# Optimization experiments

Measured on AMD Instinct MI355X. Metric: run time of the kernel, lower is better.

Reference implementation:

```python
import jax, jax.numpy as jnp
import numpy as np

N_OP, N_TASK, N_TENSOR, N_LINK = 4096, 64, 32768, 1024
N_PLACE = N_OP * N_TASK
NODE_H, EDGE_H = 64, 8
RAW_OP, RAW_TASK, RAW_E = 256, 64, 16
ETYPES = ['link', 'prev', 'succ', 'place', 'serve']
N_LAYERS = 6


def setup_inputs():
    key = jax.random.key(0)
    ks = jax.random.split(key, 20)
    f = jnp.float32
    def w(k, shape, fan_in):
        return jax.random.normal(k, shape, f) / np.sqrt(fan_in)
    return {
        'op_feats': jax.random.normal(ks[0], (N_OP, RAW_OP), f),
        'task_feats': jax.random.normal(ks[1], (N_TASK, RAW_TASK), f),
        'tensor_feats': jax.random.normal(ks[2], (N_TENSOR, RAW_E), f),
        'link_feats': jax.random.normal(ks[3], (N_LINK, RAW_E), f),
        'place_feats': jax.random.normal(ks[4], (N_PLACE, RAW_E), f),
        'prev_src': jax.random.randint(ks[5], (N_TENSOR,), 0, N_OP, jnp.int32),
        'prev_dst': jax.random.randint(ks[6], (N_TENSOR,), 0, N_OP, jnp.int32),
        'link_src': jax.random.randint(ks[7], (N_LINK,), 0, N_TASK, jnp.int32),
        'link_dst': jax.random.randint(ks[8], (N_LINK,), 0, N_TASK, jnp.int32),
        'op_W': w(ks[9], (RAW_OP, NODE_H), RAW_OP),
        'op_b': jnp.zeros((NODE_H,), f),
        'task_W': w(ks[10], (RAW_TASK, NODE_H), RAW_TASK),
        'task_b': jnp.zeros((NODE_H,), f),
        # 5 per-etype edge-trans Dense layers, all raw edge dim = RAW_E
        'eW': w(ks[11], (5, RAW_E, EDGE_H), RAW_E),
        'eb': jnp.zeros((5, EDGE_H), f),
        # GConv Dense per (etype, layer): input = NODE_H + EDGE_H = 72
        'gW': w(ks[12], (5, N_LAYERS, NODE_H + EDGE_H, NODE_H), NODE_H + EDGE_H),
        'gb': jnp.zeros((5, N_LAYERS, NODE_H), f),
        'final_W': w(ks[13], (NODE_H + EDGE_H + NODE_H, 1), NODE_H + EDGE_H + NODE_H),
        'final_b': jnp.zeros((1,), f),
    }


def _mean_agg(msgs, dst, num_segments):
    s = jax.ops.segment_sum(msgs, dst, num_segments=num_segments)
    cnt = jax.ops.segment_sum(jnp.ones((msgs.shape[0], 1), msgs.dtype), dst,
                              num_segments=num_segments)
    return s / jnp.maximum(cnt, 1.0)


def _forward(op_feats, task_feats, tensor_feats, link_feats, place_feats,
             op_W, op_b, task_W, task_b, eW, eb, gW, gb, final_W, final_b,
             prev_src, prev_dst, link_src, link_dst):
    elu = jax.nn.elu
    op = elu(op_feats @ op_W + op_b)      # [N_OP, 64]
    task = elu(task_feats @ task_W + task_b)  # [N_TASK, 64]

    raw_e = {'link': link_feats, 'prev': tensor_feats, 'succ': tensor_feats,
             'place': place_feats, 'serve': place_feats}
    ef = {et: elu(raw_e[et] @ eW[i] + eb[i]) for i, et in enumerate(ETYPES)}

    # place edges: complete bipartite, row-major by op (matches final reshape)
    place_src = jnp.repeat(jnp.arange(N_OP, dtype=jnp.int32), N_TASK)
    place_dst = jnp.tile(jnp.arange(N_TASK, dtype=jnp.int32), N_OP)

    # etype -> (src_idx, dst_idx, src_kind, dst_kind)
    topo = {
        'link':  (link_src, link_dst, 'task', 'task'),
        'prev':  (prev_src, prev_dst, 'op', 'op'),
        'succ':  (prev_dst, prev_src, 'op', 'op'),
        'place': (place_src, place_dst, 'op', 'task'),
        'serve': (place_dst, place_src, 'task', 'op'),
    }
    n_nodes = {'op': N_OP, 'task': N_TASK}

    for l in range(N_LAYERS):
        op_dst, task_dst = [], []
        for i, et in enumerate(ETYPES):
            sidx, didx, skind, dkind = topo[et]
            src = op if skind == 'op' else task
            # gather-concat-Dense per edge: [E, 72] @ [72, 64]
            m = jnp.concatenate([src[sidx], ef[et]], axis=1) @ gW[i, l] + gb[i, l]
            o = _mean_agg(m, didx, n_nodes[dkind])
            (op_dst if dkind == 'op' else task_dst).append(o)
        op = elu(op + sum(op_dst) / len(op_dst))
        task = elu(task + sum(task_dst) / len(task_dst))

    # final per-place-edge score: concat(src op, place edge feat, dst task)
    d = jnp.concatenate([op[place_src], ef['place'], task[place_dst]], axis=1)
    d = d @ final_W + final_b  # [N_PLACE, 1]
    return jnp.reshape(d[:, 0], (N_OP, N_TASK))


def reference(op_feats, task_feats, tensor_feats, link_feats, place_feats,
              prev_src, prev_dst, link_src, link_dst,
              op_W, op_b, task_W, task_b, eW, eb, gW, gb, final_W, final_b):
    return _forward(op_feats, task_feats, tensor_feats, link_feats, place_feats,
                    op_W, op_b, task_W, task_b, eW, eb, gW, gb, final_W, final_b,
                    prev_src, prev_dst, link_src, link_dst)
```

## Files before the change

kernel.cpp:

```cpp
#include <hip/hip_runtime.h>
#include <math.h>

#define NOP 4096
#define NTASK 64
#define NTENSOR 32768
#define NLINK 1024
#define NPLACE (NOP*NTASK)
#define CAP 64
#define NOPB 512

enum : int {
  O_CNT_PREV  = 0,
  O_CNT_SUCC  = O_CNT_PREV + NOP,
  O_CNT_LINK  = O_CNT_SUCC + NOP,
  O_SEF_PREV  = O_CNT_LINK + 64,
  O_SEF_SUCC  = O_SEF_PREV + NOP*8,
  O_SEF_LINK  = O_SEF_SUCC + NOP*8,
  O_SEF_PLACE = O_SEF_LINK + 64*8,
  O_SEF_SERVE = O_SEF_PLACE + 64*8,
  O_OP_A      = O_SEF_SERVE + NOP*8,
  O_OP_B      = O_OP_A + NOP*64,
  O_TASK_A    = O_OP_B + NOP*64,
  O_TASK_B    = O_TASK_A + 64*64,
  O_BPLACE    = O_TASK_B + 64*64,
  O_AOP       = O_BPLACE + NPLACE,
  O_CVEC      = O_AOP + NOP,
  O_MOPP      = O_CVEC + 64,
  O_MTPP      = O_MOPP + 2*512*64,
  O_SPLP      = O_MTPP + 2*4*64,
  O_CSRP_PREV = O_SPLP + 256*512,
  O_CSRP_SUCC = O_CSRP_PREV + NOP*CAP,
  O_CSRP_LINK = O_CSRP_SUCC + NOP*CAP,
  O_EFS_PREV  = O_CSRP_LINK + 64*CAP,
  O_EFS_SUCC  = O_EFS_PREV + NOP*CAP*8,
  O_EFS_LINK  = O_EFS_SUCC + NOP*CAP*8,
  O_TOTAL     = O_EFS_LINK + 64*CAP*8
};

__device__ __forceinline__ float elu1(float x) { return x > 0.f ? x : expm1f(x); }

__device__ __forceinline__ void fma4(float4& a, const float s, const float4 w) {
  a.x = fmaf(s, w.x, a.x);
  a.y = fmaf(s, w.y, a.y);
  a.z = fmaf(s, w.z, a.z);
  a.w = fmaf(s, w.w, a.w);
}

__global__ __launch_bounds__(256) void k_embed(
    const float* __restrict__ opA, const float* __restrict__ opW, const float* __restrict__ opb,
    const float* __restrict__ taskA, const float* __restrict__ taskW, const float* __restrict__ taskb,
    float* __restrict__ ws)
{
  const int tid = threadIdx.x;
  const int bid = blockIdx.x;
  if (bid < 256) {
    __shared__ float sW[8192];
    __shared__ float sA[16*260];
    __shared__ float4 red[256];
    const int obase = bid * 16;
    for (int i = tid; i < 4096; i += 256) {
      const int o = i >> 8, k = i & 255;
      sA[o*260 + k] = opA[(size_t)(obase + o)*256 + k];
    }
    const int o = tid >> 4, hq = tid & 15, h0 = hq*4;
    float4 acc = *(const float4*)&opb[h0];
    for (int half = 0; half < 2; ++half) {
      __syncthreads();
      for (int i = tid*4; i < 8192; i += 1024)
        *(float4*)&sW[i] = *(const float4*)&opW[half*8192 + i];
      __syncthreads();
      const float* a = &sA[o*260 + half*128];
      for (int k = 0; k < 128; ++k)
        fma4(acc, a[k], *(const float4*)&sW[k*64 + h0]);
    }
    acc.x = elu1(acc.x); acc.y = elu1(acc.y); acc.z = elu1(acc.z); acc.w = elu1(acc.w);
    *(float4*)&ws[O_OP_A + (size_t)(obase + o)*64 + h0] = acc;
    red[tid] = acc;
    __syncthreads();
    if (tid < 16) {
      float4 s = make_float4(0.f,0.f,0.f,0.f);
      for (int g = 0; g < 16; ++g) {
        float4 v = red[g*16 + tid];
        s.x += v.x; s.y += v.y; s.z += v.z; s.w += v.w;
      }
      *(float4*)&ws[O_MOPP + bid*64 + tid*4] = s;
    }
  } else {
    __shared__ float sA[64*65];
    __shared__ float sW[64*64];
    __shared__ float4 red[256];
    int* ib = (int*)ws;
    for (int i = tid; i < NOP*2 + 64; i += 256) ib[O_CNT_PREV + i] = 0;
    for (int i = tid; i < 4096; i += 256) {
      const int t = i >> 6, k = i & 63;
      sA[t*65 + k] = taskA[i];
    }
    for (int i = tid*4; i < 4096; i += 1024)
      *(float4*)&sW[i] = *(const float4*)&taskW[i];
    __syncthreads();
    const int og = tid >> 4, hq = tid & 15, h0 = hq*4;
    float4 msum = make_float4(0.f,0.f,0.f,0.f);
    for (int tg = 0; tg < 4; ++tg) {
      const int t = tg*16 + og;
      float4 acc = *(const float4*)&taskb[h0];
      const float* a = &sA[t*65];
      for (int k = 0; k < 64; ++k)
        fma4(acc, a[k], *(const float4*)&sW[k*64 + h0]);
      acc.x = elu1(acc.x); acc.y = elu1(acc.y); acc.z = elu1(acc.z); acc.w = elu1(acc.w);
      *(float4*)&ws[O_TASK_A + t*64 + h0] = acc;
      msum.x += acc.x; msum.y += acc.y; msum.z += acc.z; msum.w += acc.w;
    }
    red[tid] = msum;
    __syncthreads();
    if (tid < 16) {
      float4 s = make_float4(0.f,0.f,0.f,0.f);
      for (int g = 0; g < 16; ++g) {
        float4 v = red[g*16 + tid];
        s.x += v.x; s.y += v.y; s.z += v.z; s.w += v.w;
      }
      *(float4*)&ws[O_MTPP + tid*4] = s;
    }
  }
}

__global__ __launch_bounds__(256) void k_edge_place(
    const float* __restrict__ tensor_feats, const float* __restrict__ link_feats,
    const float* __restrict__ place_feats,
    const int* __restrict__ prev_src, const int* __restrict__ prev_dst,
    const int* __restrict__ link_src, const int* __restrict__ link_dst,
    const float* __restrict__ eW, const float* __restrict__ eb,
    const float* __restrict__ finalW, float* __restrict__ ws)
{
  const int tid = threadIdx.x;
  const int bid = blockIdx.x;
  int* ib = (int*)ws;
  if (bid < 128) {
    __shared__ float sEW[384];
    __shared__ float sEB[24];
    for (int i = tid; i < 384; i += 256) sEW[i] = eW[i];
    if (tid < 24) sEB[tid] = eb[tid];
    __syncthreads();
    const int e = bid*256 + tid;
    float raw[16];
    *(float4*)&raw[0]  = *(const float4*)&tensor_feats[(size_t)e*16 + 0];
    *(float4*)&raw[4]  = *(const float4*)&tensor_feats[(size_t)e*16 + 4];
    *(float4*)&raw[8]  = *(const float4*)&tensor_feats[(size_t)e*16 + 8];
    *(float4*)&raw[12] = *(const float4*)&tensor_feats[(size_t)e*16 + 12];
    float efp[8], efs[8];
#pragma unroll
    for (int c = 0; c < 8; ++c) { efp[c] = sEB[8+c]; efs[c] = sEB[16+c]; }
#pragma unroll
    for (int k = 0; k < 16; ++k) {
      const float a = raw[k];
#pragma unroll
      for (int c = 0; c < 8; ++c) {
        efp[c] = fmaf(a, sEW[128 + k*8 + c], efp[c]);
        efs[c] = fmaf(a, sEW[256 + k*8 + c], efs[c]);
      }
    }
#pragma unroll
    for (int c = 0; c < 8; ++c) { efp[c] = elu1(efp[c]); efs[c] = elu1(efs[c]); }
    const int pd = prev_dst[e], ps = prev_src[e];
    {
      int pos = atomicAdd(&ib[O_CNT_PREV + pd], 1);
      if (pos < CAP) {
        ib[O_CSRP_PREV + pd*CAP + pos] = ps;
        float* dst = ws + O_EFS_PREV + ((size_t)pd*CAP + pos)*8;
        *(float4*)&dst[0] = make_float4(efp[0],efp[1],efp[2],efp[3]);
        *(float4*)&dst[4] = make_float4(efp[4],efp[5],efp[6],efp[7]);
      }
    }
    {
      int pos = atomicAdd(&ib[O_CNT_SUCC + ps], 1);
      if (pos < CAP) {
        ib[O_CSRP_SUCC + ps*CAP + pos] = pd;
        float* dst = ws + O_EFS_SUCC + ((size_t)ps*CAP + pos)*8;
        *(float4*)&dst[0] = make_float4(efs[0],efs[1],efs[2],efs[3]);
        *(float4*)&dst[4] = make_float4(efs[4],efs[5],efs[6],efs[7]);
      }
    }
    if (e < NLINK) {
      float rl[16];
      *(float4*)&rl[0]  = *(const float4*)&link_feats[(size_t)e*16 + 0];
      *(float4*)&rl[4]  = *(const float4*)&link_feats[(size_t)e*16 + 4];
      *(float4*)&rl[8]  = *(const float4*)&link_feats[(size_t)e*16 + 8];
      *(float4*)&rl[12] = *(const float4*)&link_feats[(size_t)e*16 + 12];
      float efl[8];
#pragma unroll
      for (int c = 0; c < 8; ++c) efl[c] = sEB[c];
#pragma unroll
      for (int k = 0; k < 16; ++k) {
        const float a = rl[k];
#pragma unroll
        for (int c = 0; c < 8; ++c) efl[c] = fmaf(a, sEW[k*8 + c], efl[c]);
      }
      const int ld = link_dst[e];
      int pos = atomicAdd(&ib[O_CNT_LINK + ld], 1);
      if (pos < CAP) {
        ib[O_CSRP_LINK + ld*CAP + pos] = link_src[e];
        float* dst = ws + O_EFS_LINK + ((size_t)ld*CAP + pos)*8;
        *(float4*)&dst[0] = make_float4(elu1(efl[0]),elu1(efl[1]),elu1(efl[2]),elu1(efl[3]));
        *(float4*)&dst[4] = make_float4(elu1(efl[4]),elu1(efl[5]),elu1(efl[6]),elu1(efl[7]));
      }
    }
  } else {
    __shared__ float sW3[128], sW4[128], sB3[8], sB4[8], sW1[8];
    __shared__ float pl[512];
    const int pbid = bid - 128;
    if (tid < 128) { sW3[tid] = eW[3*128 + tid]; sW4[tid] = eW[4*128 + tid]; }
    if (tid < 8) { sB3[tid] = eb[24+tid]; sB4[tid] = eb[32+tid]; sW1[tid] = finalW[64+tid]; }
    for (int i = tid; i < 512; i += 256) pl[i] = 0.f;
    __syncthreads();
    const int lane = tid & 63;
    const int wave = (pbid*256 + tid) >> 6;
    float pacc[8];
#pragma unroll
    for (int c = 0; c < 8; ++c) pacc[c] = 0.f;
    float* bplace = ws + O_BPLACE;
    float* sserve = ws + O_SEF_SERVE;
    for (int j = 0; j < 4; ++j) {
      const int i = wave*4 + j;
      const int e = i*64 + lane;
      float raw[16];
      *(float4*)&raw[0]  = *(const float4*)&place_feats[(size_t)e*16 + 0];
      *(float4*)&raw[4]  = *(const float4*)&place_feats[(size_t)e*16 + 4];
      *(float4*)&raw[8]  = *(const float4*)&place_feats[(size_t)e*16 + 8];
      *(float4*)&raw[12] = *(const float4*)&place_feats[(size_t)e*16 + 12];
      float efp[8], efs[8];
#pragma unroll
      for (int c = 0; c < 8; ++c) { efp[c] = sB3[c]; efs[c] = sB4[c]; }
#pragma unroll
      for (int k = 0; k < 16; ++k) {
        const float a = raw[k];
#pragma unroll
        for (int c = 0; c < 8; ++c) {
          efp[c] = fmaf(a, sW3[k*8 + c], efp[c]);
          efs[c] = fmaf(a, sW4[k*8 + c], efs[c]);
        }
      }
      float bp = 0.f;
#pragma unroll
      for (int c = 0; c < 8; ++c) {
        efp[c] = elu1(efp[c]);
        efs[c] = elu1(efs[c]);
        bp = fmaf(efp[c], sW1[c], bp);
        pacc[c] += efp[c];
      }
      bplace[e] = bp;
#pragma unroll
      for (int c = 0; c < 8; ++c) {
        float v = efs[c];
        for (int m = 32; m >= 1; m >>= 1) v += __shfl_xor(v, m, 64);
        if (lane == 0) sserve[i*8 + c] = v;
      }
    }
#pragma unroll
    for (int c = 0; c < 8; ++c) atomicAdd(&pl[lane*8 + c], pacc[c]);
    __syncthreads();
    for (int i = tid; i < 512; i += 256) ws[O_SPLP + pbid*512 + i] = pl[i];
  }
}

__global__ __launch_bounds__(256) void k_layer(
    const int l,
    const float* __restrict__ gW, const float* __restrict__ gb,
    const float* __restrict__ finalW,
    const float* __restrict__ op_in, float* __restrict__ op_out,
    const float* __restrict__ task_in, float* __restrict__ task_out,
    float* __restrict__ ws)
{
  __shared__ float smem[12544];
  const int tid = threadIdx.x;
  const int bid = blockIdx.x;
  const int* ib = (const int*)ws;
  const int rpar = l & 1, wpar = 1 - rpar;

  if (bid < NOPB) {
    float* sWp    = smem;
    float* sWs    = smem + 4608;
    float* sWeS   = smem + 9216;
    float* vp     = smem + 9728;
    float* sums_p = smem + 9984;
    float* sums_s = smem + 10528;
    float* sGB    = smem + 11072;
    float* sef    = smem + 11200;
    float* mop    = smem + 11392;
    int* idxp_s   = (int*)(smem + 11456);
    int* idxs_s   = (int*)(smem + 11968);
    int* cp_s     = (int*)(smem + 12480);
    int* cs_s     = (int*)(smem + 12488);

    const int obase = bid*8;
    const float* gWprev  = gW + (size_t)((6  + l)*72)*64;
    const float* gWsucc  = gW + (size_t)((12 + l)*72)*64;
    const float* gWserve = gW + (size_t)((24 + l)*72)*64;

    for (int i = tid*4; i < 4608; i += 1024) {
      *(float4*)&sWp[i] = *(const float4*)&gWprev[i];
      *(float4*)&sWs[i] = *(const float4*)&gWsucc[i];
    }
    if (tid*4 < 512) *(float4*)&sWeS[tid*4] = *(const float4*)&gWserve[4096 + tid*4];
    if (tid < 8) cp_s[tid] = ib[O_CNT_PREV + obase + tid];
    else if (tid < 16) cs_s[tid-8] = ib[O_CNT_SUCC + obase + (tid-8)];
    for (int i = tid; i < 8*CAP; i += 256) {
      const int o = i >> 6, j = i & 63;
      if (j < ib[O_CNT_PREV + obase + o]) idxp_s[i] = ib[O_CSRP_PREV + (obase+o)*CAP + j];
      if (j < ib[O_CNT_SUCC + obase + o]) idxs_s[i] = ib[O_CSRP_SUCC + (obase+o)*CAP + j];
    }
    if (tid < 128) sGB[tid] = (tid < 64) ? gb[(6+l)*64 + tid] : gb[(12+l)*64 + (tid-64)];
    if (tid < 64) mop[tid] = 0.f;
    if (l == 0) {
      if (tid < 128) {
        const bool isP = (tid < 64);
        const int t2 = tid & 63;
        const int o = t2 >> 3, c = t2 & 7;
        const int cnt = min(ib[(isP ? O_CNT_PREV : O_CNT_SUCC) + obase + o], CAP);
        const float* efs = ws + (isP ? O_EFS_PREV : O_EFS_SUCC) + ((size_t)(obase+o)*CAP)*8;
        float s0 = 0.f, s1 = 0.f;
        int j = 0;
        for (; j+1 < cnt; j += 2) { s0 += efs[j*8+c]; s1 += efs[j*8+8+c]; }
        if (j < cnt) s0 += efs[j*8+c];
        const float s = s0 + s1;
        sef[tid] = s;
        ws[(isP ? O_SEF_PREV : O_SEF_SUCC) + obase*8 + t2] = s;
      } else if (tid < 192) {
        sef[tid] = ws[O_SEF_SERVE + obase*8 + (tid-128)];
      }
    } else {
      if (tid < 64)       sef[tid] = ws[O_SEF_PREV + obase*8 + tid];
      else if (tid < 128) sef[tid] = ws[O_SEF_SUCC + obase*8 + (tid-64)];
      else if (tid < 192) sef[tid] = ws[O_SEF_SERVE + obase*8 + (tid-128)];
    }
    {
      const int col = tid & 63, g = tid >> 6;
      const float* mtpp = ws + O_MTPP + rpar*256;
      const int nst = (l == 0) ? 1 : 4;
      float acc = (g == 0) ? gb[(24+l)*64 + col] : 0.f;
      for (int kk = 0; kk < 16; ++kk) {
        const int k = g*16 + kk;
        float mt = 0.f;
        for (int s = 0; s < nst; ++s) mt += mtpp[s*64 + k];
        acc = fmaf(mt*(1.f/64.f), gWserve[k*64 + col], acc);
      }
      vp[g*64 + col] = acc;
    }
    __syncthreads();

    const int wv = tid >> 6, lane = tid & 63;
#pragma unroll
    for (int oo = 0; oo < 2; ++oo) {
      const int o = 2*wv + oo;
      {
        const int pe = min(cp_s[o], CAP);
        float s0=0.f,s1=0.f,s2=0.f,s3=0.f;
        int p = 0;
        for (; p+3 < pe; p += 4) {
          s0 += op_in[(size_t)idxp_s[o*CAP+p  ]*64 + lane];
          s1 += op_in[(size_t)idxp_s[o*CAP+p+1]*64 + lane];
          s2 += op_in[(size_t)idxp_s[o*CAP+p+2]*64 + lane];
          s3 += op_in[(size_t)idxp_s[o*CAP+p+3]*64 + lane];
        }
        for (; p < pe; ++p) s0 += op_in[(size_t)idxp_s[o*CAP+p]*64 + lane];
        sums_p[o*68 + lane] = (s0+s1)+(s2+s3);
      }
      {
        const int pe = min(cs_s[o], CAP);
        float s0=0.f,s1=0.f,s2=0.f,s3=0.f;
        int p = 0;
        for (; p+3 < pe; p += 4) {
          s0 += op_in[(size_t)idxs_s[o*CAP+p  ]*64 + lane];
          s1 += op_in[(size_t)idxs_s[o*CAP+p+1]*64 + lane];
          s2 += op_in[(size_t)idxs_s[o*CAP+p+2]*64 + lane];
          s3 += op_in[(size_t)idxs_s[o*CAP+p+3]*64 + lane];
        }
        for (; p < pe; ++p) s0 += op_in[(size_t)idxs_s[o*CAP+p]*64 + lane];
        sums_s[o*68 + lane] = (s0+s1)+(s2+s3);
      }
    }

    const int oL = tid >> 5, c = (tid & 31)*2;
    const int d  = obase + oL;
    float up0 = 0.f, up1 = 0.f, us0 = 0.f, us1 = 0.f;
    const int cp = cp_s[oL];
    if (cp > 0) {
      float a0 = 0.f, a1 = 0.f;
      for (int k = 0; k < 64; ++k) {
        const float sk = sums_p[oL*68 + k];
        const float2 wv2 = *(const float2*)&sWp[k*64 + c];
        a0 = fmaf(sk, wv2.x, a0);
        a1 = fmaf(sk, wv2.y, a1);
      }
#pragma unroll
      for (int cc = 0; cc < 8; ++cc) {
        const float ev = sef[oL*8 + cc];
        const float2 wv2 = *(const float2*)&sWp[4096 + cc*64 + c];
        a0 = fmaf(ev, wv2.x, a0);
        a1 = fmaf(ev, wv2.y, a1);
      }
      const float r = 1.f/(float)cp;
      up0 = fmaf(a0, r, sGB[c]);
      up1 = fmaf(a1, r, sGB[c+1]);
    }
    const int cs = cs_s[oL];
    if (cs > 0) {
      float a0 = 0.f, a1 = 0.f;
      for (int k = 0; k < 64; ++k) {
        const float sk = sums_s[oL*68 + k];
        const float2 wv2 = *(const float2*)&sWs[k*64 + c];
        a0 = fmaf(sk, wv2.x, a0);
        a1 = fmaf(sk, wv2.y, a1);
      }
#pragma unroll
      for (int cc = 0; cc < 8; ++cc) {
        const float ev = sef[64 + oL*8 + cc];
        const float2 wv2 = *(const float2*)&sWs[4096 + cc*64 + c];
        a0 = fmaf(ev, wv2.x, a0);
        a1 = fmaf(ev, wv2.y, a1);
      }
      const float r = 1.f/(float)cs;
      us0 = fmaf(a0, r, sGB[64 + c]);
      us1 = fmaf(a1, r, sGB[64 + c + 1]);
    }
    float g0, g1;
    {
      const float2 v0 = *(const float2*)&vp[c];
      const float2 v1 = *(const float2*)&vp[64 + c];
      const float2 v2 = *(const float2*)&vp[128 + c];
      const float2 v3 = *(const float2*)&vp[192 + c];
      g0 = (v0.x + v1.x) + (v2.x + v3.x);
      g1 = (v0.y + v1.y) + (v2.y + v3.y);
#pragma unroll
      for (int cc = 0; cc < 8; ++cc) {
        const float ev = sef[128 + oL*8 + cc] * (1.f/64.f);
        const float2 wv2 = *(const float2*)&sWeS[cc*64 + c];
        g0 = fmaf(ev, wv2.x, g0);
        g1 = fmaf(ev, wv2.y, g1);
      }
    }
    const float2 x = *(const float2*)&op_in[(size_t)d*64 + c];
    const float r0 = elu1(x.x + (up0 + us0 + g0)*(1.f/3.f));
    const float r1 = elu1(x.y + (up1 + us1 + g1)*(1.f/3.f));
    if (l < 5) {
      float2 xo; xo.x = r0; xo.y = r1;
      *(float2*)&op_out[(size_t)d*64 + c] = xo;
      atomicAdd(&mop[c],   r0);
      atomicAdd(&mop[c+1], r1);
      __syncthreads();
      if (tid < 64) ws[O_MOPP + wpar*32768 + bid*64 + tid] = mop[tid];
    } else {
      float av = r0*finalW[c] + r1*finalW[c+1];
      av += __shfl_xor(av, 1, 64);
      av += __shfl_xor(av, 2, 64);
      av += __shfl_xor(av, 4, 64);
      av += __shfl_xor(av, 8, 64);
      av += __shfl_xor(av, 16, 64);
      if ((tid & 31) == 0) ws[O_AOP + d] = av;
    }
  } else {
    const int tbase = (bid - NOPB)*16;
    float* sTask  = smem;
    float* sW0    = smem + 4096;
    float* sWe3   = smem + 8704;
    float* vpl    = smem + 9216;
    float* mo4    = smem + 9472;
    float* sums_l = smem + 9728;
    float* sGB0   = smem + 10816;
    float* sefl   = smem + 10880;
    float* sefpl  = smem + 11008;
    float* mtp    = smem + 11136;
    int* idxl_s   = (int*)(smem + 11200);
    int* cl_s     = (int*)(smem + 12224);

    const float* gWlink  = gW + (size_t)(l*72)*64;
    const float* gWplace = gW + (size_t)((18 + l)*72)*64;

    {
      const int col = tid & 63, g = tid >> 6;
      const float* mopp = ws + O_MOPP + rpar*32768;
      const int nso = (l == 0) ? 256 : 512;
      float a0=0.f,a1=0.f,a2=0.f,a3=0.f,a4=0.f,a5=0.f,a6=0.f,a7=0.f;
      for (int s = g; s < nso; s += 32) {
        a0 += mopp[(s+0 )*64 + col];
        a1 += mopp[(s+4 )*64 + col];
        a2 += mopp[(s+8 )*64 + col];
        a3 += mopp[(s+12)*64 + col];
        a4 += mopp[(s+16)*64 + col];
        a5 += mopp[(s+20)*64 + col];
        a6 += mopp[(s+24)*64 + col];
        a7 += mopp[(s+28)*64 + col];
      }
      mo4[g*64 + col] = ((a0+a1)+(a2+a3)) + ((a4+a5)+(a6+a7));
    }
    for (int i = tid*4; i < 4096; i += 1024)
      *(float4*)&sTask[i] = *(const float4*)&task_in[i];
    for (int i = tid*4; i < 4608; i += 1024)
      *(float4*)&sW0[i] = *(const float4*)&gWlink[i];
    if (tid*4 < 512) *(float4*)&sWe3[tid*4] = *(const float4*)&gWplace[4096 + tid*4];
    if (tid < 16) cl_s[tid] = ib[O_CNT_LINK + tbase + tid];
    for (int i = tid; i < 16*CAP; i += 256) {
      const int t = i >> 6, j = i & 63;
      if (j < ib[O_CNT_LINK + tbase + t]) idxl_s[i] = ib[O_CSRP_LINK + (tbase+t)*CAP + j];
    }
    if (tid < 64) { sGB0[tid] = gb[l*64 + tid]; mtp[tid] = 0.f; }
    if (l == 0) {
      if (tid < 128) {
        const int t = tid >> 3, c = tid & 7;
        const int cnt = min(ib[O_CNT_LINK + tbase + t], CAP);
        const float* efs = ws + O_EFS_LINK + ((size_t)(tbase+t)*CAP)*8;
        float s0 = 0.f, s1 = 0.f;
        int j = 0;
        for (; j+1 < cnt; j += 2) { s0 += efs[j*8+c]; s1 += efs[j*8+8+c]; }
        if (j < cnt) s0 += efs[j*8+c];
        const float s = s0 + s1;
        sefl[tid] = s;
        ws[O_SEF_LINK + tbase*8 + tid] = s;
      } else {
        const int idx = tid - 128;
        float s0=0.f,s1=0.f,s2=0.f,s3=0.f;
        for (int r = 0; r < 256; r += 4) {
          s0 += ws[O_SPLP + (r+0)*512 + tbase*8 + idx];
          s1 += ws[O_SPLP + (r+1)*512 + tbase*8 + idx];
          s2 += ws[O_SPLP + (r+2)*512 + tbase*8 + idx];
          s3 += ws[O_SPLP + (r+3)*512 + tbase*8 + idx];
        }
        const float s = (s0+s1)+(s2+s3);
        sefpl[idx] = s;
        ws[O_SEF_PLACE + tbase*8 + idx] = s;
      }
    } else {
      if (tid < 128) sefl[tid] = ws[O_SEF_LINK + tbase*8 + tid];
      else sefpl[tid - 128] = ws[O_SEF_PLACE + tbase*8 + (tid - 128)];
    }
    __syncthreads();
    {
      const int col = tid & 63, g = tid >> 6;
      float acc = (g == 0) ? gb[(18+l)*64 + col] : 0.f;
      for (int kk = 0; kk < 16; ++kk) {
        const int k = g*16 + kk;
        const float mok = (mo4[k] + mo4[64+k]) + (mo4[128+k] + mo4[192+k]);
        acc = fmaf(mok*(1.f/4096.f), gWplace[k*64 + col], acc);
      }
      vpl[g*64 + col] = acc;
    }
    __syncthreads();

    const int wv = tid >> 6, lane = tid & 63;
#pragma unroll
    for (int tt = 0; tt < 4; ++tt) {
      const int t = 4*wv + tt;
      const int pe = min(cl_s[t], CAP);
      float s0=0.f,s1=0.f,s2=0.f,s3=0.f;
      int p = 0;
      for (; p+3 < pe; p += 4) {
        s0 += sTask[idxl_s[t*CAP+p  ]*64 + lane];
        s1 += sTask[idxl_s[t*CAP+p+1]*64 + lane];
        s2 += sTask[idxl_s[t*CAP+p+2]*64 + lane];
        s3 += sTask[idxl_s[t*CAP+p+3]*64 + lane];
      }
      for (; p < pe; ++p) s0 += sTask[idxl_s[t*CAP+p]*64 + lane];
      sums_l[t*68 + lane] = (s0+s1)+(s2+s3);
    }

    const int tL = tid >> 4, h0 = (tid & 15)*4;
    const int tG = tbase + tL;
    float4 ul = make_float4(0.f,0.f,0.f,0.f);
    const int cl2 = cl_s[tL];
    if (cl2 > 0) {
      float4 a = make_float4(0.f,0.f,0.f,0.f);
      for (int k = 0; k < 64; ++k)
        fma4(a, sums_l[tL*68 + k], *(const float4*)&sW0[k*64 + h0]);
#pragma unroll
      for (int cc = 0; cc < 8; ++cc)
        fma4(a, sefl[tL*8 + cc], *(const float4*)&sW0[4096 + cc*64 + h0]);
      const float r = 1.f/(float)cl2;
      ul.x = fmaf(a.x, r, sGB0[h0+0]);
      ul.y = fmaf(a.y, r, sGB0[h0+1]);
      ul.z = fmaf(a.z, r, sGB0[h0+2]);
      ul.w = fmaf(a.w, r, sGB0[h0+3]);
    }
    float4 uq;
    {
      const float4 v0 = *(const float4*)&vpl[h0];
      const float4 v1 = *(const float4*)&vpl[64 + h0];
      const float4 v2 = *(const float4*)&vpl[128 + h0];
      const float4 v3 = *(const float4*)&vpl[192 + h0];
      uq.x = (v0.x+v1.x)+(v2.x+v3.x);
      uq.y = (v0.y+v1.y)+(v2.y+v3.y);
      uq.z = (v0.z+v1.z)+(v2.z+v3.z);
      uq.w = (v0.w+v1.w)+(v2.w+v3.w);
#pragma unroll
      for (int cc = 0; cc < 8; ++cc)
        fma4(uq, sefpl[tL*8 + cc]*(1.f/4096.f), *(const float4*)&sWe3[cc*64 + h0]);
    }
    float4 x = *(const float4*)&sTask[tG*64 + h0];
    x.x = elu1(x.x + (ul.x + uq.x)*0.5f);
    x.y = elu1(x.y + (ul.y + uq.y)*0.5f);
    x.z = elu1(x.z + (ul.z + uq.z)*0.5f);
    x.w = elu1(x.w + (ul.w + uq.w)*0.5f);
    if (l < 5) {
      *(float4*)&task_out[(size_t)tG*64 + h0] = x;
      atomicAdd(&mtp[h0+0], x.x);
      atomicAdd(&mtp[h0+1], x.y);
      atomicAdd(&mtp[h0+2], x.z);
      atomicAdd(&mtp[h0+3], x.w);
      __syncthreads();
      if (tid < 64) ws[O_MTPP + wpar*256 + (bid - NOPB)*64 + tid] = mtp[tid];
    } else {
      const float4 fw = *(const float4*)&finalW[72 + h0];
      float cv = x.x*fw.x + x.y*fw.y + x.z*fw.z + x.w*fw.w;
      cv += __shfl_xor(cv, 1, 64);
      cv += __shfl_xor(cv, 2, 64);
      cv += __shfl_xor(cv, 4, 64);
      cv += __shfl_xor(cv, 8, 64);
      if ((tid & 15) == 0) ws[O_CVEC + tG] = cv;
    }
  }
}

__global__ __launch_bounds__(256) void k_final(
    const float* __restrict__ ws, const float* __restrict__ finalb,
    float* __restrict__ out)
{
  const int e4 = (blockIdx.x*256 + threadIdx.x)*4;
  const int i = e4 >> 6;
  const int t = e4 & 63;
  const float a = ws[O_AOP + i];
  const float fb = finalb[0];
  const float4 bp = *(const float4*)&ws[O_BPLACE + e4];
  const float4 cv = *(const float4*)&ws[O_CVEC + t];
  float4 o4;
  o4.x = a + bp.x + cv.x + fb;
  o4.y = a + bp.y + cv.y + fb;
  o4.z = a + bp.z + cv.z + fb;
  o4.w = a + bp.w + cv.w + fb;
  *(float4*)&out[e4] = o4;
}

extern "C" void kernel_launch(void* const* d_in, const int* in_sizes, int n_in,
                              void* d_out, int out_size, void* d_ws, size_t ws_size,
                              hipStream_t stream)
{
  (void)in_sizes; (void)n_in; (void)out_size;
  if (ws_size < (size_t)O_TOTAL * sizeof(float)) return;

  const float* op_feats     = (const float*)d_in[0];
  const float* task_feats   = (const float*)d_in[1];
  const float* tensor_feats = (const float*)d_in[2];
  const float* link_feats   = (const float*)d_in[3];
  const float* place_feats  = (const float*)d_in[4];
  const int*   prev_src     = (const int*)d_in[5];
  const int*   prev_dst     = (const int*)d_in[6];
  const int*   link_src     = (const int*)d_in[7];
  const int*   link_dst     = (const int*)d_in[8];
  const float* op_W         = (const float*)d_in[9];
  const float* op_b         = (const float*)d_in[10];
  const float* task_W       = (const float*)d_in[11];
  const float* task_b       = (const float*)d_in[12];
  const float* eW           = (const float*)d_in[13];
  const float* eb           = (const float*)d_in[14];
  const float* gW           = (const float*)d_in[15];
  const float* gb           = (const float*)d_in[16];
  const float* finalW       = (const float*)d_in[17];
  const float* finalb       = (const float*)d_in[18];
  float* w = (float*)d_ws;
  float* out = (float*)d_out;

  k_embed<<<257, 256, 0, stream>>>(op_feats, op_W, op_b, task_feats, task_W, task_b, w);
  k_edge_place<<<384, 256, 0, stream>>>(tensor_feats, link_feats, place_feats,
                                        prev_src, prev_dst, link_src, link_dst,
                                        eW, eb, finalW, w);

  for (int l = 0; l < 6; ++l) {
    const float* oin  = w + ((l & 1) ? O_OP_B : O_OP_A);
    float*       oout = w + ((l & 1) ? O_OP_A : O_OP_B);
    const float* tin  = w + ((l & 1) ? O_TASK_B : O_TASK_A);
    float*       tout = w + ((l & 1) ? O_TASK_A : O_TASK_B);
    k_layer<<<NOPB + 4, 256, 0, stream>>>(l, gW, gb, finalW, oin, oout, tin, tout, w);
  }

  k_final<<<256, 256, 0, stream>>>(w, finalb, out);
}
```

Baseline: 194.9 us.

## Merge op embedding with edge/place prep, overlap weight loads with gathers

Measured after the change: 222.2 us. 1.14x slower.

```diff
diff --git a/kernel.cpp b/kernel.cpp
--- a/kernel.cpp
+++ b/kernel.cpp
@@ -46,17 +46,73 @@
   a.w = fmaf(s, w.w, a.w);
 }
 
-__global__ __launch_bounds__(256) void k_embed(
-    const float* __restrict__ opA, const float* __restrict__ opW, const float* __restrict__ opb,
-    const float* __restrict__ taskA, const float* __restrict__ taskW, const float* __restrict__ taskb,
-    float* __restrict__ ws)
+__global__ __launch_bounds__(256) void k_pre(
+    const float* __restrict__ taskA, const float* __restrict__ taskW,
+    const float* __restrict__ taskb, float* __restrict__ ws)
 {
   const int tid = threadIdx.x;
   const int bid = blockIdx.x;
+  if (bid > 0) {
+    int* ib = (int*)ws;
+    for (int i = (bid - 1)*1024 + tid*4; i < NOP*2 + 64; i += 8192) {
+      ib[O_CNT_PREV + i+0] = 0;
+      ib[O_CNT_PREV + i+1] = 0;
+      ib[O_CNT_PREV + i+2] = 0;
+      ib[O_CNT_PREV + i+3] = 0;
+    }
+    return;
+  }
+  __shared__ float sA[64*65];
+  __shared__ float sW[64*64];
+  __shared__ float4 red[256];
+  for (int i = tid; i < 4096; i += 256) {
+    const int t = i >> 6, k = i & 63;
+    sA[t*65 + k] = taskA[i];
+  }
+  for (int i = tid*4; i < 4096; i += 1024)
+    *(float4*)&sW[i] = *(const float4*)&taskW[i];
+  __syncthreads();
+  const int og = tid >> 4, hq = tid & 15, h0 = hq*4;
+  float4 msum = make_float4(0.f,0.f,0.f,0.f);
+  for (int tg = 0; tg < 4; ++tg) {
+    const int t = tg*16 + og;
+    float4 acc = *(const float4*)&taskb[h0];
+    const float* a = &sA[t*65];
+    for (int k = 0; k < 64; ++k)
+      fma4(acc, a[k], *(const float4*)&sW[k*64 + h0]);
+    acc.x = elu1(acc.x); acc.y = elu1(acc.y); acc.z = elu1(acc.z); acc.w = elu1(acc.w);
+    *(float4*)&ws[O_TASK_A + t*64 + h0] = acc;
+    msum.x += acc.x; msum.y += acc.y; msum.z += acc.z; msum.w += acc.w;
+  }
+  red[tid] = msum;
+  __syncthreads();
+  if (tid < 16) {
+    float4 s = make_float4(0.f,0.f,0.f,0.f);
+    for (int g = 0; g < 16; ++g) {
+      float4 v = red[g*16 + tid];
+      s.x += v.x; s.y += v.y; s.z += v.z; s.w += v.w;
+    }
+    *(float4*)&ws[O_MTPP + tid*4] = s;
+  }
+}
+
+__global__ __launch_bounds__(256) void k_prep(
+    const float* __restrict__ opA, const float* __restrict__ opW, const float* __restrict__ opb,
+    const float* __restrict__ tensor_feats, const float* __restrict__ link_feats,
+    const float* __restrict__ place_feats,
+    const int* __restrict__ prev_src, const int* __restrict__ prev_dst,
+    const int* __restrict__ link_src, const int* __restrict__ link_dst,
+    const float* __restrict__ eW, const float* __restrict__ eb,
+    const float* __restrict__ finalW, float* __restrict__ ws)
+{
+  __shared__ float smem[13376];
+  const int tid = threadIdx.x;
+  const int bid = blockIdx.x;
+  int* ib = (int*)ws;
   if (bid < 256) {
-    __shared__ float sW[8192];
-    __shared__ float sA[16*260];
-    __shared__ float4 red[256];
+    float* sW = smem;
+    float* sA = smem + 8192;
+    float4* red = (float4*)(smem + 12352);
     const int obase = bid * 16;
     for (int i = tid; i < 4096; i += 256) {
       const int o = i >> 8, k = i & 255;
@@ -85,62 +141,13 @@
       }
       *(float4*)&ws[O_MOPP + bid*64 + tid*4] = s;
     }
-  } else {
-    __shared__ float sA[64*65];
-    __shared__ float sW[64*64];
-    __shared__ float4 red[256];
-    int* ib = (int*)ws;
-    for (int i = tid; i < NOP*2 + 64; i += 256) ib[O_CNT_PREV + i] = 0;
-    for (int i = tid; i < 4096; i += 256) {
-      const int t = i >> 6, k = i & 63;
-      sA[t*65 + k] = taskA[i];
-    }
-    for (int i = tid*4; i < 4096; i += 1024)
-      *(float4*)&sW[i] = *(const float4*)&taskW[i];
-    __syncthreads();
-    const int og = tid >> 4, hq = tid & 15, h0 = hq*4;
-    float4 msum = make_float4(0.f,0.f,0.f,0.f);
-    for (int tg = 0; tg < 4; ++tg) {
-      const int t = tg*16 + og;
-      float4 acc = *(const float4*)&taskb[h0];
-      const float* a = &sA[t*65];
-      for (int k = 0; k < 64; ++k)
-        fma4(acc, a[k], *(const float4*)&sW[k*64 + h0]);
-      acc.x = elu1(acc.x); acc.y = elu1(acc.y); acc.z = elu1(acc.z); acc.w = elu1(acc.w);
-      *(float4*)&ws[O_TASK_A + t*64 + h0] = acc;
-      msum.x += acc.x; msum.y += acc.y; msum.z += acc.z; msum.w += acc.w;
-    }
-    red[tid] = msum;
-    __syncthreads();
-    if (tid < 16) {
-      float4 s = make_float4(0.f,0.f,0.f,0.f);
-      for (int g = 0; g < 16; ++g) {
-        float4 v = red[g*16 + tid];
-        s.x += v.x; s.y += v.y; s.z += v.z; s.w += v.w;
-      }
-      *(float4*)&ws[O_MTPP + tid*4] = s;
-    }
-  }
-}
-
-__global__ __launch_bounds__(256) void k_edge_place(
-    const float* __restrict__ tensor_feats, const float* __restrict__ link_feats,
-    const float* __restrict__ place_feats,
-    const int* __restrict__ prev_src, const int* __restrict__ prev_dst,
-    const int* __restrict__ link_src, const int* __restrict__ link_dst,
-    const float* __restrict__ eW, const float* __restrict__ eb,
-    const float* __restrict__ finalW, float* __restrict__ ws)
-{
-  const int tid = threadIdx.x;
-  const int bid = blockIdx.x;
-  int* ib = (int*)ws;
-  if (bid < 128) {
-    __shared__ float sEW[384];
-    __shared__ float sEB[24];
+  } else if (bid < 384) {
+    float* sEW = smem;
+    float* sEB = smem + 384;
     for (int i = tid; i < 384; i += 256) sEW[i] = eW[i];
     if (tid < 24) sEB[tid] = eb[tid];
     __syncthreads();
-    const int e = bid*256 + tid;
+    const int e = (bid - 256)*256 + tid;
     float raw[16];
     *(float4*)&raw[0]  = *(const float4*)&tensor_feats[(size_t)e*16 + 0];
     *(float4*)&raw[4]  = *(const float4*)&tensor_feats[(size_t)e*16 + 4];
@@ -163,7 +170,7 @@
     const int pd = prev_dst[e], ps = prev_src[e];
     {
       int pos = atomicAdd(&ib[O_CNT_PREV + pd], 1);
-      if (pos < CAP) {
+      if (pos >= 0 && pos < CAP) {
         ib[O_CSRP_PREV + pd*CAP + pos] = ps;
         float* dst = ws + O_EFS_PREV + ((size_t)pd*CAP + pos)*8;
         *(float4*)&dst[0] = make_float4(efp[0],efp[1],efp[2],efp[3]);
@@ -172,7 +179,7 @@
     }
     {
       int pos = atomicAdd(&ib[O_CNT_SUCC + ps], 1);
-      if (pos < CAP) {
+      if (pos >= 0 && pos < CAP) {
         ib[O_CSRP_SUCC + ps*CAP + pos] = pd;
         float* dst = ws + O_EFS_SUCC + ((size_t)ps*CAP + pos)*8;
         *(float4*)&dst[0] = make_float4(efs[0],efs[1],efs[2],efs[3]);
@@ -196,7 +203,7 @@
       }
       const int ld = link_dst[e];
       int pos = atomicAdd(&ib[O_CNT_LINK + ld], 1);
-      if (pos < CAP) {
+      if (pos >= 0 && pos < CAP) {
         ib[O_CSRP_LINK + ld*CAP + pos] = link_src[e];
         float* dst = ws + O_EFS_LINK + ((size_t)ld*CAP + pos)*8;
         *(float4*)&dst[0] = make_float4(elu1(efl[0]),elu1(efl[1]),elu1(efl[2]),elu1(efl[3]));
@@ -204,9 +211,13 @@
       }
     }
   } else {
-    __shared__ float sW3[128], sW4[128], sB3[8], sB4[8], sW1[8];
-    __shared__ float pl[512];
-    const int pbid = bid - 128;
+    float* sW3 = smem;
+    float* sW4 = smem + 128;
+    float* sB3 = smem + 256;
+    float* sB4 = smem + 264;
+    float* sW1 = smem + 272;
+    float* pl  = smem + 280;
+    const int pbid = bid - 384;
     if (tid < 128) { sW3[tid] = eW[3*128 + tid]; sW4[tid] = eW[4*128 + tid]; }
     if (tid < 8) { sB3[tid] = eb[24+tid]; sB4[tid] = eb[32+tid]; sW1[tid] = finalW[64+tid]; }
     for (int i = tid; i < 512; i += 256) pl[i] = 0.f;
@@ -295,11 +306,17 @@
     const float* gWsucc  = gW + (size_t)((12 + l)*72)*64;
     const float* gWserve = gW + (size_t)((24 + l)*72)*64;
 
-    for (int i = tid*4; i < 4608; i += 1024) {
-      *(float4*)&sWp[i] = *(const float4*)&gWprev[i];
-      *(float4*)&sWs[i] = *(const float4*)&gWsucc[i];
-    }
-    if (tid*4 < 512) *(float4*)&sWeS[tid*4] = *(const float4*)&gWserve[4096 + tid*4];
+    float4 wreg[10];
+#pragma unroll
+    for (int j = 0; j < 10; ++j) {
+      const int i = tid*4 + j*1024;
+      if (i < 9728) {
+        const float* src = (i < 4608) ? &gWprev[i]
+                         : (i < 9216) ? &gWsucc[i - 4608]
+                                      : &gWserve[4096 + (i - 9216)];
+        wreg[j] = *(const float4*)src;
+      }
+    }
     if (tid < 8) cp_s[tid] = ib[O_CNT_PREV + obase + tid];
     else if (tid < 16) cs_s[tid-8] = ib[O_CNT_SUCC + obase + (tid-8)];
     for (int i = tid; i < 8*CAP; i += 256) {
@@ -310,22 +327,7 @@
     if (tid < 128) sGB[tid] = (tid < 64) ? gb[(6+l)*64 + tid] : gb[(12+l)*64 + (tid-64)];
     if (tid < 64) mop[tid] = 0.f;
     if (l == 0) {
-      if (tid < 128) {
-        const bool isP = (tid < 64);
-        const int t2 = tid & 63;
-        const int o = t2 >> 3, c = t2 & 7;
-        const int cnt = min(ib[(isP ? O_CNT_PREV : O_CNT_SUCC) + obase + o], CAP);
-        const float* efs = ws + (isP ? O_EFS_PREV : O_EFS_SUCC) + ((size_t)(obase+o)*CAP)*8;
-        float s0 = 0.f, s1 = 0.f;
-        int j = 0;
-        for (; j+1 < cnt; j += 2) { s0 += efs[j*8+c]; s1 += efs[j*8+8+c]; }
-        if (j < cnt) s0 += efs[j*8+c];
-        const float s = s0 + s1;
-        sef[tid] = s;
-        ws[(isP ? O_SEF_PREV : O_SEF_SUCC) + obase*8 + t2] = s;
-      } else if (tid < 192) {
-        sef[tid] = ws[O_SEF_SERVE + obase*8 + (tid-128)];
-      }
+      if (tid >= 128 && tid < 192) sef[tid] = ws[O_SEF_SERVE + obase*8 + (tid-128)];
     } else {
       if (tid < 64)       sef[tid] = ws[O_SEF_PREV + obase*8 + tid];
       else if (tid < 128) sef[tid] = ws[O_SEF_SUCC + obase*8 + (tid-64)];
@@ -350,33 +352,69 @@
 #pragma unroll
     for (int oo = 0; oo < 2; ++oo) {
       const int o = 2*wv + oo;
-      {
-        const int pe = min(cp_s[o], CAP);
+      const int pep = min(cp_s[o], CAP);
+      const int pes = min(cs_s[o], CAP);
+      const int* ip = &idxp_s[o*CAP];
+      const int* iq = &idxs_s[o*CAP];
+      float p0=0.f,p1=0.f,p2=0.f,p3=0.f,q0=0.f,q1=0.f,q2=0.f,q3=0.f;
+      int p = 0, q = 0;
+      while (p+3 < pep && q+3 < pes) {
+        const int a0=ip[p],a1=ip[p+1],a2=ip[p+2],a3=ip[p+3];
+        const int b0=iq[q],b1=iq[q+1],b2=iq[q+2],b3=iq[q+3];
+        p0 += op_in[(size_t)a0*64 + lane];
+        p1 += op_in[(size_t)a1*64 + lane];
+        p2 += op_in[(size_t)a2*64 + lane];
+        p3 += op_in[(size_t)a3*64 + lane];
+        q0 += op_in[(size_t)b0*64 + lane];
+        q1 += op_in[(size_t)b1*64 + lane];
+        q2 += op_in[(size_t)b2*64 + lane];
+        q3 += op_in[(size_t)b3*64 + lane];
+        p += 4; q += 4;
+      }
+      for (; p+3 < pep; p += 4) {
+        const int a0=ip[p],a1=ip[p+1],a2=ip[p+2],a3=ip[p+3];
+        p0 += op_in[(size_t)a0*64 + lane];
+        p1 += op_in[(size_t)a1*64 + lane];
+        p2 += op_in[(size_t)a2*64 + lane];
+        p3 += op_in[(size_t)a3*64 + lane];
+      }
+      for (; q+3 < pes; q += 4) {
+        const int b0=iq[q],b1=iq[q+1],b2=iq[q+2],b3=iq[q+3];
+        q0 += op_in[(size_t)b0*64 + lane];
+        q1 += op_in[(size_t)b1*64 + lane];
+        q2 += op_in[(size_t)b2*64 + lane];
+        q3 += op_in[(size_t)b3*64 + lane];
+      }
+      for (; p < pep; ++p) p0 += op_in[(size_t)ip[p]*64 + lane];
+      for (; q < pes; ++q) q0 += op_in[(size_t)iq[q]*64 + lane];
+      sums_p[o*68 + lane] = (p0+p1)+(p2+p3);
+      sums_s[o*68 + lane] = (q0+q1)+(q2+q3);
+    }
+    if (l == 0) {
+      if (tid < 128) {
+        const bool isP = (tid < 64);
+        const int t2 = tid & 63;
+        const int o = t2 >> 3, c = t2 & 7;
+        const int cnt = min(isP ? cp_s[o] : cs_s[o], CAP);
+        const float* efs = ws + (isP ? O_EFS_PREV : O_EFS_SUCC) + ((size_t)(obase+o)*CAP)*8;
         float s0=0.f,s1=0.f,s2=0.f,s3=0.f;
-        int p = 0;
-        for (; p+3 < pe; p += 4) {
-          s0 += op_in[(size_t)idxp_s[o*CAP+p  ]*64 + lane];
-          s1 += op_in[(size_t)idxp_s[o*CAP+p+1]*64 + lane];
-          s2 += op_in[(size_t)idxp_s[o*CAP+p+2]*64 + lane];
-          s3 += op_in[(size_t)idxp_s[o*CAP+p+3]*64 + lane];
+        int j = 0;
+        for (; j+3 < cnt; j += 4) {
+          s0 += efs[j*8+c]; s1 += efs[(j+1)*8+c];
+          s2 += efs[(j+2)*8+c]; s3 += efs[(j+3)*8+c];
         }
-        for (; p < pe; ++p) s0 += op_in[(size_t)idxp_s[o*CAP+p]*64 + lane];
-        sums_p[o*68 + lane] = (s0+s1)+(s2+s3);
-      }
-      {
-        const int pe = min(cs_s[o], CAP);
-        float s0=0.f,s1=0.f,s2=0.f,s3=0.f;
-        int p = 0;
-        for (; p+3 < pe; p += 4) {
-          s0 += op_in[(size_t)idxs_s[o*CAP+p  ]*64 + lane];
-          s1 += op_in[(size_t)idxs_s[o*CAP+p+1]*64 + lane];
-          s2 += op_in[(size_t)idxs_s[o*CAP+p+2]*64 + lane];
-          s3 += op_in[(size_t)idxs_s[o*CAP+p+3]*64 + lane];
-        }
-        for (; p < pe; ++p) s0 += op_in[(size_t)idxs_s[o*CAP+p]*64 + lane];
-        sums_s[o*68 + lane] = (s0+s1)+(s2+s3);
-      }
-    }
+        for (; j < cnt; ++j) s0 += efs[j*8+c];
+        const float s = (s0+s1)+(s2+s3);
+        sef[tid] = s;
+        ws[(isP ? O_SEF_PREV : O_SEF_SUCC) + obase*8 + t2] = s;
+      }
+    }
+#pragma unroll
+    for (int j = 0; j < 10; ++j) {
+      const int i = tid*4 + j*1024;
+      if (i < 9728) *(float4*)&smem[i] = wreg[j];
+    }
+    __syncthreads();
 
     const int oL = tid >> 5, c = (tid & 31)*2;
     const int d  = obase + oL;
@@ -665,10 +703,11 @@
   float* w = (float*)d_ws;
   float* out = (float*)d_out;
 
-  k_embed<<<257, 256, 0, stream>>>(op_feats, op_W, op_b, task_feats, task_W, task_b, w);
-  k_edge_place<<<384, 256, 0, stream>>>(tensor_feats, link_feats, place_feats,
-                                        prev_src, prev_dst, link_src, link_dst,
-                                        eW, eb, finalW, w);
+  k_pre<<<9, 256, 0, stream>>>(task_feats, task_W, task_b, w);
+  k_prep<<<640, 256, 0, stream>>>(op_feats, op_W, op_b,
+                                  tensor_feats, link_feats, place_feats,
+                                  prev_src, prev_dst, link_src, link_dst,
+                                  eW, eb, finalW, w);
 
   for (int l = 0; l < 6; ++l) {
     const float* oin  = w + ((l & 1) ? O_OP_B : O_OP_A);
```
